# Kernel tuning notes

Measured on AMD Instinct MI355X. Metric: run time of the kernel, lower is better.

The kernel has to match this reference:

```python
import jax, jax.numpy as jnp
import numpy as np

LN_EPS = 1e-5


def setup_inputs() -> dict:
    key = jax.random.key(0)
    ks = jax.random.split(key, 5)
    B, P, D = 2048, 54, 512
    scale = 1.0 / np.sqrt(D)  # mimic nn.Linear init scale
    return {
        "x": jax.random.normal(ks[0], (B, P, D), dtype=jnp.float32),
        "W1": jax.random.normal(ks[1], (P, D, D), dtype=jnp.float32) * scale,
        "b1": jax.random.normal(ks[2], (P, D), dtype=jnp.float32) * scale,
        "W2": jax.random.normal(ks[3], (P, D, D), dtype=jnp.float32) * scale,
        "b2": jax.random.normal(ks[4], (P, D), dtype=jnp.float32) * scale,
        "gamma": jnp.ones((D,), dtype=jnp.float32),
        "beta": jnp.zeros((D,), dtype=jnp.float32),
    }


def reference(x, W1, b1, W2, b2, gamma, beta):
    # Per-patch 2-layer MLP, vectorized over the patch dim P (grouped GEMM).
    # nn.Linear applies y = x @ W.T + b; W here stored as [P, out, in] -> contract on 'e' (in).
    h = jnp.einsum("bpe,pde->bpd", x, W1) + b1[None, :, :]
    h = jax.nn.gelu(h, approximate=False)  # torch nn.GELU default = exact erf
    o = jnp.einsum("bpe,pde->bpd", h, W2) + b2[None, :, :]
    # dropout is identity in eval/deterministic baseline
    res = o + x
    mu = jnp.mean(res, axis=-1, keepdims=True)
    var = jnp.var(res, axis=-1, keepdims=True)
    out = (res - mu) * jax.lax.rsqrt(var + LN_EPS) * gamma + beta
    return out
```

## Files before the change

### kernel.cpp

```cpp
#include <hip/hip_runtime.h>
#include <hip/hip_bf16.h>
#include <math.h>


#define B_DIM 2048
#define P_DIM 54
#define D_DIM 512

typedef __attribute__((ext_vector_type(8))) short short8;
typedef __attribute__((ext_vector_type(4))) float floatx4;

__device__ __forceinline__ unsigned short f2bf(float f) {
    union { float f; unsigned int i; } c; c.f = f;
    unsigned int r = c.i + 0x7FFFu + ((c.i >> 16) & 1u);
    return (unsigned short)(r >> 16);
}

__device__ __forceinline__ unsigned int f2bf2(float a, float b) {
    __hip_bfloat162 h2 = __float22bfloat162_rn(make_float2(a, b));
    unsigned int u; __builtin_memcpy(&u, &h2, 4); return u;
}

__device__ __forceinline__ void gload_lds16(const unsigned short* g, unsigned short* l) {
    __builtin_amdgcn_global_load_lds((const __attribute__((address_space(1))) void*)g,
                                     (__attribute__((address_space(3))) void*)l,
                                     16, 0, 0);
}

__global__ __launch_bounds__(256) void gemm1_gelu(
    const float* __restrict__ x,
    const float* __restrict__ W1,
    const float* __restrict__ b1,
    unsigned short* __restrict__ h)
{
    __shared__ __align__(16) unsigned short sA[128 * 32];
    __shared__ __align__(16) unsigned short sB[128 * 32];

    const int tid   = threadIdx.x;
    const int wave  = tid >> 6;
    const int lane  = tid & 63;
    const int quad  = lane >> 4;
    const int colid = lane & 15;

    const int m0 = blockIdx.x * 128;
    const int n0 = blockIdx.y * 128;
    const int p  = blockIdx.z;

    const long xstride = (long)P_DIM * D_DIM;
    const float* xp  = x  + (long)m0 * xstride + (long)p * D_DIM;
    const float* w1p = W1 + ((long)p * D_DIM + n0) * D_DIM;

    const int srow = tid >> 3;
    const int sch  = (tid & 7) * 4;

    floatx4 acc[4][4];
#pragma unroll
    for (int i = 0; i < 4; i++)
#pragma unroll
        for (int j = 0; j < 4; j++)
            acc[i][j] = (floatx4){0.f, 0.f, 0.f, 0.f};

    const int wm = (wave & 1) * 64;
    const int wn = (wave >> 1) * 64;

    for (int kt = 0; kt < D_DIM; kt += 32) {
        float4 va[4], vb[4];
#pragma unroll
        for (int q = 0; q < 4; q++) {
            const int r = q * 32 + srow;
            va[q] = *(const float4*)(xp  + (long)r * xstride + kt + sch);
            vb[q] = *(const float4*)(w1p + (long)r * D_DIM   + kt + sch);
        }
        __syncthreads();
#pragma unroll
        for (int q = 0; q < 4; q++) {
            const int r = q * 32 + srow;
            uint2 pa, pb;
            pa.x = f2bf2(va[q].x, va[q].y); pa.y = f2bf2(va[q].z, va[q].w);
            pb.x = f2bf2(vb[q].x, vb[q].y); pb.y = f2bf2(vb[q].z, vb[q].w);
            *(uint2*)&sA[r * 32 + sch] = pa;
            *(uint2*)&sB[r * 32 + sch] = pb;
        }
        __syncthreads();

        short8 a[4], b[4];
#pragma unroll
        for (int i = 0; i < 4; i++) {
            a[i] = *(const short8*)&sA[(wm + i * 16 + colid) * 32 + quad * 8];
            b[i] = *(const short8*)&sB[(wn + i * 16 + colid) * 32 + quad * 8];
        }
#pragma unroll
        for (int i = 0; i < 4; i++)
#pragma unroll
            for (int j = 0; j < 4; j++)
                acc[i][j] = __builtin_amdgcn_mfma_f32_16x16x32_bf16(a[i], b[j], acc[i][j], 0, 0, 0);
    }

#pragma unroll
    for (int j = 0; j < 4; j++) {
        const int n = n0 + wn + j * 16 + colid;
        const float bias = b1[p * D_DIM + n];
#pragma unroll
        for (int i = 0; i < 4; i++) {
#pragma unroll
            for (int r = 0; r < 4; r++) {
                const int m = m0 + wm + i * 16 + quad * 4 + r;
                float v = acc[i][j][r] + bias;
                v = 0.5f * v * (1.0f + erff(v * 0.70710678118654752f));
                h[(long)m * xstride + (long)p * D_DIM + n] = f2bf(v);
            }
        }
    }
}

__global__ __launch_bounds__(512) void gemm2_ln(
    const unsigned short* __restrict__ h,
    const float* __restrict__ W2,
    const float* __restrict__ b2,
    const float* __restrict__ x,
    const float* __restrict__ gamma,
    const float* __restrict__ beta,
    float* __restrict__ out)
{
    __shared__ __align__(16) unsigned short sH[64 * 32];
    __shared__ __align__(16) unsigned short sW[512 * 32];
    __shared__ float red1[64 * 8];
    __shared__ float red2[64 * 8];
    __shared__ float sMu[64], sRs[64];
    __shared__ float sG[512], sBt[512];

    const int tid   = threadIdx.x;
    const int wave  = tid >> 6;
    const int lane  = tid & 63;
    const int quad  = lane >> 4;
    const int colid = lane & 15;

    const int m0 = blockIdx.x * 64;
    const int p  = blockIdx.y;

    sG[tid]  = gamma[tid];
    sBt[tid] = beta[tid];

    const long rstride = (long)P_DIM * D_DIM;
    const unsigned short* hp = h + (long)m0 * rstride + (long)p * D_DIM;
    const float*         w2p = W2 + (long)p * D_DIM * D_DIM;

    const int srow = tid >> 3;
    const int sch  = (tid & 7) * 4;
    const int hrow = lane >> 2;
    const int hoff = (lane & 3) * 8;

    floatx4 acc[4][4];
#pragma unroll
    for (int i = 0; i < 4; i++)
#pragma unroll
        for (int j = 0; j < 4; j++)
            acc[i][j] = (floatx4){0.f, 0.f, 0.f, 0.f};

    const int wn = wave * 64;

    for (int kt = 0; kt < D_DIM; kt += 32) {
        float4 vw[8];
#pragma unroll
        for (int q = 0; q < 8; q++) {
            const int r = q * 64 + srow;
            vw[q] = *(const float4*)(w2p + (long)r * D_DIM + kt + sch);
        }
        __syncthreads();
#pragma unroll
        for (int q = 0; q < 8; q++) {
            const int r = q * 64 + srow;
            uint2 pw;
            pw.x = f2bf2(vw[q].x, vw[q].y); pw.y = f2bf2(vw[q].z, vw[q].w);
            *(uint2*)&sW[r * 32 + sch] = pw;
        }
        if (wave < 4) {
            const int r = wave * 16;
            gload_lds16(hp + (long)(r + hrow) * rstride + kt + hoff, &sH[r * 32]);
        }
        __syncthreads();

        short8 a[4], b[4];
#pragma unroll
        for (int i = 0; i < 4; i++) {
            a[i] = *(const short8*)&sH[(i * 16 + colid) * 32 + quad * 8];
            b[i] = *(const short8*)&sW[(wn + i * 16 + colid) * 32 + quad * 8];
        }
#pragma unroll
        for (int i = 0; i < 4; i++)
#pragma unroll
            for (int j = 0; j < 4; j++)
                acc[i][j] = __builtin_amdgcn_mfma_f32_16x16x32_bf16(a[i], b[j], acc[i][j], 0, 0, 0);
    }

    const float* xp = x + (long)m0 * rstride + (long)p * D_DIM;
#pragma unroll
    for (int j = 0; j < 4; j++) {
        const int n = wn + j * 16 + colid;
        const float bias = b2[p * D_DIM + n];
#pragma unroll
        for (int i = 0; i < 4; i++) {
#pragma unroll
            for (int r = 0; r < 4; r++) {
                const int row = i * 16 + quad * 4 + r;
                acc[i][j][r] += bias + xp[(long)row * rstride + n];
            }
        }
    }

#pragma unroll
    for (int i = 0; i < 4; i++) {
#pragma unroll
        for (int r = 0; r < 4; r++) {
            float s1 = 0.f, s2 = 0.f;
#pragma unroll
            for (int j = 0; j < 4; j++) {
                const float v = acc[i][j][r];
                s1 += v; s2 += v * v;
            }
#pragma unroll
            for (int off = 1; off < 16; off <<= 1) {
                s1 += __shfl_xor(s1, off, 16);
                s2 += __shfl_xor(s2, off, 16);
            }
            if (colid == 0) {
                const int row = i * 16 + quad * 4 + r;
                red1[row * 8 + wave] = s1;
                red2[row * 8 + wave] = s2;
            }
        }
    }
    __syncthreads();
    if (tid < 64) {
        float s1 = 0.f, s2 = 0.f;
#pragma unroll
        for (int w = 0; w < 8; w++) { s1 += red1[tid * 8 + w]; s2 += red2[tid * 8 + w]; }
        const float mu  = s1 * (1.0f / (float)D_DIM);
        const float var = s2 * (1.0f / (float)D_DIM) - mu * mu;
        sMu[tid] = mu;
        sRs[tid] = rsqrtf(var + 1e-5f);
    }
    __syncthreads();

    float* op = out + (long)m0 * rstride + (long)p * D_DIM;
#pragma unroll
    for (int j = 0; j < 4; j++) {
        const int n = wn + j * 16 + colid;
        const float g = sG[n], bt = sBt[n];
#pragma unroll
        for (int i = 0; i < 4; i++) {
#pragma unroll
            for (int r = 0; r < 4; r++) {
                const int row = i * 16 + quad * 4 + r;
                const float v = (acc[i][j][r] - sMu[row]) * sRs[row] * g + bt;
                op[(long)row * rstride + n] = v;
            }
        }
    }
}

extern "C" void kernel_launch(void* const* d_in, const int* in_sizes, int n_in,
                              void* d_out, int out_size, void* d_ws, size_t ws_size,
                              hipStream_t stream) {
    const float* x     = (const float*)d_in[0];
    const float* W1    = (const float*)d_in[1];
    const float* b1    = (const float*)d_in[2];
    const float* W2    = (const float*)d_in[3];
    const float* b2    = (const float*)d_in[4];
    const float* gamma = (const float*)d_in[5];
    const float* beta  = (const float*)d_in[6];
    float* out = (float*)d_out;
    unsigned short* h = (unsigned short*)d_ws;

    dim3 gridA(B_DIM / 128, D_DIM / 128, P_DIM);
    gemm1_gelu<<<gridA, 256, 0, stream>>>(x, W1, b1, h);

    dim3 gridB(B_DIM / 64, P_DIM);
    gemm2_ln<<<gridB, 512, 0, stream>>>(h, W2, b2, x, gamma, beta, out);
}
```

Measured before the change: 897.6 us.

## Fuse both per-patch GEMMs with GELU and LayerNorm, keeping hidden in LDS

Merges the two GEMM kernels into one block per 64-row × patch tile. The bf16 x tile and then the GELU hidden activations stay in shared memory, removing the global round trip for h. Weights are pre-converted to bf16 by a separate pass each call and streamed with double-buffered direct-to-LDS loads. The large LDS footprint limits occupancy to one block per CU.

Result: faster. 786.2 us (-12.4%).

```diff
diff --git a/kernel.cpp b/kernel.cpp
--- a/kernel.cpp
+++ b/kernel.cpp
@@ -6,15 +6,10 @@
 #define B_DIM 2048
 #define P_DIM 54
 #define D_DIM 512
+#define WTILE (D_DIM * D_DIM)
 
 typedef __attribute__((ext_vector_type(8))) short short8;
 typedef __attribute__((ext_vector_type(4))) float floatx4;
-
-__device__ __forceinline__ unsigned short f2bf(float f) {
-    union { float f; unsigned int i; } c; c.f = f;
-    unsigned int r = c.i + 0x7FFFu + ((c.i >> 16) & 1u);
-    return (unsigned short)(r >> 16);
-}
 
 __device__ __forceinline__ unsigned int f2bf2(float a, float b) {
     __hip_bfloat162 h2 = __float22bfloat162_rn(make_float2(a, b));
@@ -27,31 +22,78 @@
                                      16, 0, 0);
 }
 
-__global__ __launch_bounds__(256) void gemm1_gelu(
+__global__ __launch_bounds__(256) void cvt_bf16(const float* __restrict__ src,
+                                                unsigned short* __restrict__ dst,
+                                                int n8) {
+    const int i = blockIdx.x * 256 + threadIdx.x;
+    if (i >= n8) return;
+    const float4 v0 = ((const float4*)src)[2 * i];
+    const float4 v1 = ((const float4*)src)[2 * i + 1];
+    uint4 o;
+    o.x = f2bf2(v0.x, v0.y); o.y = f2bf2(v0.z, v0.w);
+    o.z = f2bf2(v1.x, v1.y); o.w = f2bf2(v1.z, v1.w);
+    ((uint4*)dst)[i] = o;
+}
+
+__global__ __launch_bounds__(512) void mlp_fused(
     const float* __restrict__ x,
-    const float* __restrict__ W1,
+    const unsigned short* __restrict__ W1b,
     const float* __restrict__ b1,
-    unsigned short* __restrict__ h)
+    const unsigned short* __restrict__ W2b,
+    const float* __restrict__ b2,
+    const float* __restrict__ gamma,
+    const float* __restrict__ beta,
+    float* __restrict__ out)
 {
-    __shared__ __align__(16) unsigned short sA[128 * 32];
-    __shared__ __align__(16) unsigned short sB[128 * 32];
+    __shared__ __align__(16) unsigned short sXH[64 * 512];
+    __shared__ __align__(16) unsigned short sW[2][512 * 32];
+    __shared__ float red1[64 * 8];
+    __shared__ float red2[64 * 8];
+    __shared__ float sMu[64], sRs[64];
 
     const int tid   = threadIdx.x;
     const int wave  = tid >> 6;
     const int lane  = tid & 63;
     const int quad  = lane >> 4;
     const int colid = lane & 15;
-
-    const int m0 = blockIdx.x * 128;
-    const int n0 = blockIdx.y * 128;
-    const int p  = blockIdx.z;
-
-    const long xstride = (long)P_DIM * D_DIM;
-    const float* xp  = x  + (long)m0 * xstride + (long)p * D_DIM;
-    const float* w1p = W1 + ((long)p * D_DIM + n0) * D_DIM;
-
-    const int srow = tid >> 3;
-    const int sch  = (tid & 7) * 4;
+    const int wn    = wave * 64;
+
+    const int m0 = blockIdx.x * 64;
+    const int p  = blockIdx.y;
+
+    const long rstride = (long)P_DIM * D_DIM;
+    const float*          xp  = x   + (long)m0 * rstride + (long)p * D_DIM;
+    const unsigned short* w1p = W1b + (long)p * WTILE;
+    const unsigned short* w2p = W2b + (long)p * WTILE;
+
+    const int wrow0 = tid >> 2;
+    const int wk8   = (tid & 3) * 8;
+
+#pragma unroll
+    for (int r = 0; r < 4; r++)
+        gload_lds16(w1p + (r * 128 + wrow0) * D_DIM + wk8,
+                    &sW[0][r * 4096 + wave * 512]);
+
+#pragma unroll
+    for (int i = 0; i < 8; i++) {
+        const int row = i * 8 + wave;
+        const float* xrow = xp + (long)row * rstride + lane * 8;
+        const float4 v0 = *(const float4*)(xrow);
+        const float4 v1 = *(const float4*)(xrow + 4);
+        uint4 o;
+        o.x = f2bf2(v0.x, v0.y); o.y = f2bf2(v0.z, v0.w);
+        o.z = f2bf2(v1.x, v1.y); o.w = f2bf2(v1.z, v1.w);
+        const int ba = (row * 1024 + lane * 16) ^ ((wave & 7) << 4);
+        *(uint4*)((char*)sXH + ba) = o;
+    }
+
+    const int axor = (colid & 7) << 4;
+    int aoff[4], boff[4];
+#pragma unroll
+    for (int i = 0; i < 4; i++) {
+        aoff[i] = (i * 16 + colid) * 1024 + quad * 16;
+        boff[i] = (wn + i * 16 + colid) * 64 + quad * 16;
+    }
 
     floatx4 acc[4][4];
 #pragma unroll
@@ -60,140 +102,91 @@
         for (int j = 0; j < 4; j++)
             acc[i][j] = (floatx4){0.f, 0.f, 0.f, 0.f};
 
-    const int wm = (wave & 1) * 64;
-    const int wn = (wave >> 1) * 64;
-
-    for (int kt = 0; kt < D_DIM; kt += 32) {
-        float4 va[4], vb[4];
-#pragma unroll
-        for (int q = 0; q < 4; q++) {
-            const int r = q * 32 + srow;
-            va[q] = *(const float4*)(xp  + (long)r * xstride + kt + sch);
-            vb[q] = *(const float4*)(w1p + (long)r * D_DIM   + kt + sch);
-        }
+    int cur = 0;
+
+    for (int t = 0; t < 16; t++) {
         __syncthreads();
-#pragma unroll
-        for (int q = 0; q < 4; q++) {
-            const int r = q * 32 + srow;
-            uint2 pa, pb;
-            pa.x = f2bf2(va[q].x, va[q].y); pa.y = f2bf2(va[q].z, va[q].w);
-            pb.x = f2bf2(vb[q].x, vb[q].y); pb.y = f2bf2(vb[q].z, vb[q].w);
-            *(uint2*)&sA[r * 32 + sch] = pa;
-            *(uint2*)&sB[r * 32 + sch] = pb;
-        }
-        __syncthreads();
-
-        short8 a[4], b[4];
-#pragma unroll
-        for (int i = 0; i < 4; i++) {
-            a[i] = *(const short8*)&sA[(wm + i * 16 + colid) * 32 + quad * 8];
-            b[i] = *(const short8*)&sB[(wn + i * 16 + colid) * 32 + quad * 8];
-        }
-#pragma unroll
-        for (int i = 0; i < 4; i++)
-#pragma unroll
-            for (int j = 0; j < 4; j++)
-                acc[i][j] = __builtin_amdgcn_mfma_f32_16x16x32_bf16(a[i], b[j], acc[i][j], 0, 0, 0);
-    }
-
-#pragma unroll
-    for (int j = 0; j < 4; j++) {
-        const int n = n0 + wn + j * 16 + colid;
-        const float bias = b1[p * D_DIM + n];
-#pragma unroll
-        for (int i = 0; i < 4; i++) {
-#pragma unroll
-            for (int r = 0; r < 4; r++) {
-                const int m = m0 + wm + i * 16 + quad * 4 + r;
-                float v = acc[i][j][r] + bias;
-                v = 0.5f * v * (1.0f + erff(v * 0.70710678118654752f));
-                h[(long)m * xstride + (long)p * D_DIM + n] = f2bf(v);
-            }
-        }
-    }
-}
-
-__global__ __launch_bounds__(512) void gemm2_ln(
-    const unsigned short* __restrict__ h,
-    const float* __restrict__ W2,
-    const float* __restrict__ b2,
-    const float* __restrict__ x,
-    const float* __restrict__ gamma,
-    const float* __restrict__ beta,
-    float* __restrict__ out)
-{
-    __shared__ __align__(16) unsigned short sH[64 * 32];
-    __shared__ __align__(16) unsigned short sW[512 * 32];
-    __shared__ float red1[64 * 8];
-    __shared__ float red2[64 * 8];
-    __shared__ float sMu[64], sRs[64];
-    __shared__ float sG[512], sBt[512];
-
-    const int tid   = threadIdx.x;
-    const int wave  = tid >> 6;
-    const int lane  = tid & 63;
-    const int quad  = lane >> 4;
-    const int colid = lane & 15;
-
-    const int m0 = blockIdx.x * 64;
-    const int p  = blockIdx.y;
-
-    sG[tid]  = gamma[tid];
-    sBt[tid] = beta[tid];
-
-    const long rstride = (long)P_DIM * D_DIM;
-    const unsigned short* hp = h + (long)m0 * rstride + (long)p * D_DIM;
-    const float*         w2p = W2 + (long)p * D_DIM * D_DIM;
-
-    const int srow = tid >> 3;
-    const int sch  = (tid & 7) * 4;
-    const int hrow = lane >> 2;
-    const int hoff = (lane & 3) * 8;
-
-    floatx4 acc[4][4];
+        {
+            const unsigned short* nsrc = (t < 15) ? (w1p + (t + 1) * 32) : w2p;
+            unsigned short* nbuf = &sW[cur ^ 1][0];
+#pragma unroll
+            for (int r = 0; r < 4; r++)
+                gload_lds16(nsrc + (r * 128 + wrow0) * D_DIM + wk8,
+                            nbuf + r * 4096 + wave * 512);
+        }
+        const int kt2 = t * 64;
+        short8 xa[4], wb[4];
+        const char* sWc = (const char*)&sW[cur][0];
+#pragma unroll
+        for (int i = 0; i < 4; i++) {
+            xa[i] = *(const short8*)((const char*)sXH + ((aoff[i] + kt2) ^ axor));
+            wb[i] = *(const short8*)(sWc + boff[i]);
+        }
+#pragma unroll
+        for (int ni = 0; ni < 4; ni++)
+#pragma unroll
+            for (int mj = 0; mj < 4; mj++)
+                acc[ni][mj] = __builtin_amdgcn_mfma_f32_16x16x32_bf16(
+                    wb[ni], xa[mj], acc[ni][mj], 0, 0, 0);
+        cur ^= 1;
+    }
+
+    __syncthreads();
+
+#pragma unroll
+    for (int ni = 0; ni < 4; ni++) {
+        const int nbase = wn + ni * 16 + quad * 4;
+        const float4 bv = *(const float4*)(b1 + p * D_DIM + nbase);
+#pragma unroll
+        for (int mj = 0; mj < 4; mj++) {
+            const int m = mj * 16 + colid;
+            float g0 = acc[ni][mj][0] + bv.x;
+            float g1 = acc[ni][mj][1] + bv.y;
+            float g2 = acc[ni][mj][2] + bv.z;
+            float g3 = acc[ni][mj][3] + bv.w;
+            g0 = 0.5f * g0 * (1.0f + erff(g0 * 0.70710678118654752f));
+            g1 = 0.5f * g1 * (1.0f + erff(g1 * 0.70710678118654752f));
+            g2 = 0.5f * g2 * (1.0f + erff(g2 * 0.70710678118654752f));
+            g3 = 0.5f * g3 * (1.0f + erff(g3 * 0.70710678118654752f));
+            uint2 o; o.x = f2bf2(g0, g1); o.y = f2bf2(g2, g3);
+            const int ba = (m * 1024 + nbase * 2) ^ ((colid & 7) << 4);
+            *(uint2*)((char*)sXH + ba) = o;
+        }
+    }
+
 #pragma unroll
     for (int i = 0; i < 4; i++)
 #pragma unroll
         for (int j = 0; j < 4; j++)
             acc[i][j] = (floatx4){0.f, 0.f, 0.f, 0.f};
 
-    const int wn = wave * 64;
-
-    for (int kt = 0; kt < D_DIM; kt += 32) {
-        float4 vw[8];
-#pragma unroll
-        for (int q = 0; q < 8; q++) {
-            const int r = q * 64 + srow;
-            vw[q] = *(const float4*)(w2p + (long)r * D_DIM + kt + sch);
-        }
+    for (int t = 0; t < 16; t++) {
         __syncthreads();
-#pragma unroll
-        for (int q = 0; q < 8; q++) {
-            const int r = q * 64 + srow;
-            uint2 pw;
-            pw.x = f2bf2(vw[q].x, vw[q].y); pw.y = f2bf2(vw[q].z, vw[q].w);
-            *(uint2*)&sW[r * 32 + sch] = pw;
-        }
-        if (wave < 4) {
-            const int r = wave * 16;
-            gload_lds16(hp + (long)(r + hrow) * rstride + kt + hoff, &sH[r * 32]);
-        }
-        __syncthreads();
-
-        short8 a[4], b[4];
-#pragma unroll
-        for (int i = 0; i < 4; i++) {
-            a[i] = *(const short8*)&sH[(i * 16 + colid) * 32 + quad * 8];
-            b[i] = *(const short8*)&sW[(wn + i * 16 + colid) * 32 + quad * 8];
+        if (t < 15) {
+            const unsigned short* nsrc = w2p + (t + 1) * 32;
+            unsigned short* nbuf = &sW[cur ^ 1][0];
+#pragma unroll
+            for (int r = 0; r < 4; r++)
+                gload_lds16(nsrc + (r * 128 + wrow0) * D_DIM + wk8,
+                            nbuf + r * 4096 + wave * 512);
+        }
+        const int kt2 = t * 64;
+        short8 ha[4], wb[4];
+        const char* sWc = (const char*)&sW[cur][0];
+#pragma unroll
+        for (int i = 0; i < 4; i++) {
+            ha[i] = *(const short8*)((const char*)sXH + ((aoff[i] + kt2) ^ axor));
+            wb[i] = *(const short8*)(sWc + boff[i]);
         }
 #pragma unroll
         for (int i = 0; i < 4; i++)
 #pragma unroll
             for (int j = 0; j < 4; j++)
-                acc[i][j] = __builtin_amdgcn_mfma_f32_16x16x32_bf16(a[i], b[j], acc[i][j], 0, 0, 0);
-    }
-
-    const float* xp = x + (long)m0 * rstride + (long)p * D_DIM;
+                acc[i][j] = __builtin_amdgcn_mfma_f32_16x16x32_bf16(
+                    ha[i], wb[j], acc[i][j], 0, 0, 0);
+        cur ^= 1;
+    }
+
 #pragma unroll
     for (int j = 0; j < 4; j++) {
         const int n = wn + j * 16 + colid;
@@ -246,7 +239,7 @@
 #pragma unroll
     for (int j = 0; j < 4; j++) {
         const int n = wn + j * 16 + colid;
-        const float g = sG[n], bt = sBt[n];
+        const float g = gamma[n], bt = beta[n];
 #pragma unroll
         for (int i = 0; i < 4; i++) {
 #pragma unroll
@@ -270,11 +263,14 @@
     const float* gamma = (const float*)d_in[5];
     const float* beta  = (const float*)d_in[6];
     float* out = (float*)d_out;
-    unsigned short* h = (unsigned short*)d_ws;
-
-    dim3 gridA(B_DIM / 128, D_DIM / 128, P_DIM);
-    gemm1_gelu<<<gridA, 256, 0, stream>>>(x, W1, b1, h);
-
-    dim3 gridB(B_DIM / 64, P_DIM);
-    gemm2_ln<<<gridB, 512, 0, stream>>>(h, W2, b2, x, gamma, beta, out);
-}
+
+    unsigned short* W1b = (unsigned short*)d_ws;
+    unsigned short* W2b = W1b + (long)P_DIM * WTILE;
+
+    const int n8 = (P_DIM * WTILE) / 8;
+    cvt_bf16<<<n8 / 256, 256, 0, stream>>>(W1, W1b, n8);
+    cvt_bf16<<<n8 / 256, 256, 0, stream>>>(W2, W2b, n8);
+
+    dim3 grid(B_DIM / 64, P_DIM);
+    mlp_fused<<<grid, 512, 0, stream>>>(x, W1b, b1, W2b, b2, gamma, beta, out);
+}
```
